# Kernel tuning notes

Measured on AMD Instinct MI355X. Metric: run time of the kernel, lower is better.

The kernel has to match this reference:

```python
import jax, jax.numpy as jnp
import numpy as np

VERY_NEG = -100000000000.0
EPS = 1e-10
PAGERANK_LAMBDA = 0.8
FACT_SCALE = 1.0
B, E, F, LQ = 64, 1000, 4000, 30
T = 100      # trans_units
EMB = 300    # embed_units
WV = 30000   # word vocab
EV = 50007   # entity vocab (+7 specials)
GNN_LAYERS = 2


def linear(x, W, b):
    return x @ W.T + b


def lstm(x, Wih, Whh, bih, bhh):
    # torch nn.LSTM, single layer, batch_first. gate order i,f,g,o
    Bb = x.shape[0]
    H = Whh.shape[1]
    def step(carry, xt):
        h, c = carry
        g = xt @ Wih.T + h @ Whh.T + bih + bhh
        i, f, gg, o = jnp.split(g, 4, axis=-1)
        c = jax.nn.sigmoid(f) * c + jax.nn.sigmoid(i) * jnp.tanh(gg)
        h = jax.nn.sigmoid(o) * jnp.tanh(c)
        return (h, c), h
    init = (jnp.zeros((Bb, H), x.dtype), jnp.zeros((Bb, H), x.dtype))
    (h, _), ys = jax.lax.scan(step, init, jnp.swapaxes(x, 0, 1))
    return jnp.swapaxes(ys, 0, 1), h


def gather_entity(x, head_idx):
    # sparse_bmm(entity2fact_mat, x): each fact row has one nonzero at its head entity
    # x [B,E,D], head_idx [B,F] -> [B,F,D]
    return jnp.take_along_axis(x, head_idx[:, :, None], axis=1)


def scatter_fact(y, tail_idx):
    # sparse_bmm(fact2entity_mat, y): scatter-add fact rows into their tail entity
    # y [B,F,D], tail_idx [B,F] -> [B,E,D]
    Bb, Ff, D = y.shape
    seg = (jnp.arange(Bb)[:, None] * E + tail_idx).reshape(-1)
    return jax.ops.segment_sum(y.reshape(Bb * Ff, D), seg, num_segments=Bb * E).reshape(Bb, E, D)


def forward(word_emb, entity_emb, ent_W, ent_b, lstm_Wih, lstm_Whh, lstm_bih, lstm_bhh,
            q2e_W, q2e_b, e2q_W, e2q_b, e2e_W, e2e_b,
            kbh_W, kbh_b, kbt_W, kbt_b, kbs_W, kbs_b,
            q2e_adj_mat, query_text, local_entity, kb_fact_rel, head_idx, tail_idx):
    div = jnp.sqrt(jnp.asarray(T, jnp.float32))
    query_mask = (query_text != 0).astype(jnp.float32)          # [B,LQ]

    # node encoder (LSTM) over query words
    qw = word_emb[query_text]                                   # [B,LQ,EMB]
    query_hidden_emb, qh = lstm(qw, lstm_Wih, lstm_Whh, lstm_bih, lstm_bhh)
    query_node_emb = qh[:, None, :]                             # [B,1,T]

    local_fact_emb = linear(entity_emb[kb_fact_rel], ent_W, ent_b)     # [B,F,T]
    local_entity_emb = linear(entity_emb[local_entity], ent_W, ent_b)  # [B,E,T]

    # fact <-> query attention (pre-GNN weighting)
    sim = jnp.einsum('blt,bft->blf', query_hidden_emb, local_fact_emb) / div
    sim = jax.nn.softmax(sim + (1.0 - query_mask[:, :, None]) * VERY_NEG, axis=1)
    fact2query_att = jnp.einsum('blf,blt->bft', sim, query_hidden_emb)  # [B,F,T]
    Wsc = jnp.sum(fact2query_att * local_fact_emb, axis=2) / div        # [B,F]
    W_tilde = jnp.exp(Wsc - jnp.max(Wsc, axis=1, keepdims=True))        # [B,F]

    # e2f_softmax = entity2fact^T @ W_tilde : per-entity sum of W_tilde over out-facts
    e2f_softmax = scatter_fact(W_tilde[:, :, None], head_idx)[:, :, 0]
    e2f_softmax = jnp.maximum(e2f_softmax, EPS)                         # [B,E]

    pagerank_f = q2e_adj_mat                                            # [B,E]
    for i in range(GNN_LAYERS):
        next_emb = local_entity_emb
        # question -> entity
        q2e = linear(jnp.broadcast_to(query_node_emb, (B, E, T)), q2e_W[i], q2e_b[i])
        next_emb = jnp.concatenate([next_emb, q2e], axis=2)
        # entity -> fact
        e2f_emb = jax.nn.relu(linear(local_fact_emb, kbs_W[i], kbs_b[i]) +
                              gather_entity(linear(local_entity_emb, kbh_W[i], kbh_b[i]), head_idx))
        e2f_norm = W_tilde[:, :, None] * gather_entity((pagerank_f / e2f_softmax)[:, :, None], head_idx)
        e2f_emb = e2f_emb * e2f_norm                                    # [B,F,T]
        # fact -> entity
        f2e_emb = jax.nn.relu(linear(local_entity_emb, kbs_W[i], kbs_b[i]) +
                              scatter_fact(linear(e2f_emb, kbt_W[i], kbt_b[i]), tail_idx))
        pagerank_f = (PAGERANK_LAMBDA * scatter_fact(e2f_norm, tail_idx)[:, :, 0] +
                      (1.0 - PAGERANK_LAMBDA) * pagerank_f)
        next_emb = jnp.concatenate([next_emb, FACT_SCALE * f2e_emb], axis=2)  # [B,E,3T]
        # entity -> query ; entity -> entity
        query_node_emb = jnp.einsum('be,bet->bt', pagerank_f,
                                    linear(next_emb, e2q_W[i], e2q_b[i]))[:, None, :]
        local_entity_emb = jax.nn.relu(linear(next_emb, e2e_W[i], e2e_b[i]))
    return local_entity_emb, query_node_emb, pagerank_f


def setup_inputs() -> dict:
    key = jax.random.key(0)
    ks = jax.random.split(key, 24)
    def n(k, shape, s=0.05):
        return (jax.random.normal(k, shape) * s).astype(jnp.float32)
    L, K3 = GNN_LAYERS, 3 * T
    inp = {}
    inp['word_emb'] = n(ks[0], (WV, EMB), 1.0)
    inp['entity_emb'] = n(ks[1], (EV, T), 1.0)
    inp['ent_W'] = n(ks[2], (T, T)); inp['ent_b'] = jnp.zeros((T,), jnp.float32)
    inp['lstm_Wih'] = n(ks[3], (4 * T, EMB)); inp['lstm_Whh'] = n(ks[4], (4 * T, T))
    inp['lstm_bih'] = jnp.zeros((4 * T,), jnp.float32)
    inp['lstm_bhh'] = jnp.zeros((4 * T,), jnp.float32)
    inp['q2e_W'] = n(ks[5], (L, T, T)); inp['q2e_b'] = jnp.zeros((L, T), jnp.float32)
    inp['e2q_W'] = n(ks[6], (L, T, K3)); inp['e2q_b'] = jnp.zeros((L, T), jnp.float32)
    inp['e2e_W'] = n(ks[7], (L, T, K3)); inp['e2e_b'] = jnp.zeros((L, T), jnp.float32)
    inp['kbh_W'] = n(ks[8], (L, T, T)); inp['kbh_b'] = jnp.zeros((L, T), jnp.float32)
    inp['kbt_W'] = n(ks[9], (L, T, T)); inp['kbt_b'] = jnp.zeros((L, T), jnp.float32)
    inp['kbs_W'] = n(ks[10], (L, T, T)); inp['kbs_b'] = jnp.zeros((L, T), jnp.float32)
    inp['q2e_adj_mat'] = (jax.random.uniform(ks[11], (B, E)) < 0.05).astype(jnp.float32)
    inp['query_text'] = jax.random.randint(ks[12], (B, LQ), 0, WV)
    inp['local_entity'] = jax.random.randint(ks[13], (B, E), 0, EV)
    inp['kb_fact_rel'] = jax.random.randint(ks[14], (B, F), 0, EV)
    inp['head_idx'] = jax.random.randint(ks[15], (B, F), 0, E)
    inp['tail_idx'] = jax.random.randint(ks[16], (B, F), 0, E)
    return inp


def reference(word_emb, entity_emb, ent_W, ent_b, lstm_Wih, lstm_Whh, lstm_bih, lstm_bhh,
              q2e_W, q2e_b, e2q_W, e2q_b, e2e_W, e2e_b,
              kbh_W, kbh_b, kbt_W, kbt_b, kbs_W, kbs_b,
              q2e_adj_mat, query_text, local_entity, kb_fact_rel, head_idx, tail_idx):
    return forward(word_emb, entity_emb, ent_W, ent_b, lstm_Wih, lstm_Whh, lstm_bih, lstm_bhh,
                   q2e_W, q2e_b, e2q_W, e2q_b, e2e_W, e2e_b,
                   kbh_W, kbh_b, kbt_W, kbt_b, kbs_W, kbs_b,
                   q2e_adj_mat, query_text, local_entity, kb_fact_rel, head_idx, tail_idx)
```

## Files before the change

kernel.cpp:

```cpp
#include <hip/hip_runtime.h>
#include <hip/hip_bf16.h>

#define BB 64
#define EE 1000
#define FF 4000
#define LQ_ 30
#define TT 100
#define EMB_ 300
#define G4 400
#define EV_ 50007
#define VERY_NEG_ (-100000000000.0f)
#define EPS_ 1e-10f

typedef __attribute__((ext_vector_type(8))) short bf16x8;
typedef __attribute__((ext_vector_type(4))) float f32x4;

__device__ __forceinline__ float sigm(float x) { return 1.0f / (1.0f + expf(-x)); }

__device__ __forceinline__ unsigned short f2bf(float v) {
    __hip_bfloat16 h = __float2bfloat16(v);
    return *reinterpret_cast<unsigned short*>(&h);
}
__device__ __forceinline__ float bf2f(unsigned short s) {
    return __uint_as_float((unsigned)s << 16);
}

__global__ void cvt_bf16_kernel(const float* __restrict__ in, unsigned short* __restrict__ out,
                                long n4) {
    long i = (long)blockIdx.x * 256 + threadIdx.x;
    if (i < n4) {
        float4 v = ((const float4*)in)[i];
        ushort4 o;
        o.x = f2bf(v.x); o.y = f2bf(v.y); o.z = f2bf(v.z); o.w = f2bf(v.w);
        ((ushort4*)out)[i] = o;
    }
}

__global__ void transpose_kernel(const float* __restrict__ in, float* __restrict__ out,
                                 int rows, int cols) {
    int i = blockIdx.x * 256 + threadIdx.x;
    if (i < rows * cols) {
        int r = i / cols, c = i % cols;
        out[c * rows + r] = in[i];
    }
}

__global__ __launch_bounds__(256)
void xw_kernel(const float* __restrict__ word_emb, const int* __restrict__ qtext,
               const float* __restrict__ WihT, const float* __restrict__ bih,
               const float* __restrict__ bhh, float* __restrict__ xw) {
    int bs0 = blockIdx.x * 4;
    __shared__ float x[4][EMB_];
    int tid = threadIdx.x;
    for (int i = tid; i < 4 * EMB_; i += 256) {
        int s = i / EMB_, k = i % EMB_;
        x[s][k] = word_emb[(long)qtext[bs0 + s] * EMB_ + k];
    }
    __syncthreads();
    for (int g = tid; g < G4; g += 256) {
        float b0 = bih[g] + bhh[g];
        float a0 = b0, a1 = b0, a2 = b0, a3 = b0;
        #pragma unroll 4
        for (int k = 0; k < EMB_; ++k) {
            float wv = WihT[k * G4 + g];
            a0 += x[0][k] * wv; a1 += x[1][k] * wv;
            a2 += x[2][k] * wv; a3 += x[3][k] * wv;
        }
        xw[(long)(bs0 + 0) * G4 + g] = a0;
        xw[(long)(bs0 + 1) * G4 + g] = a1;
        xw[(long)(bs0 + 2) * G4 + g] = a2;
        xw[(long)(bs0 + 3) * G4 + g] = a3;
    }
}

__global__ __launch_bounds__(512)
void lstm_kernel(const float* __restrict__ xw, const float* __restrict__ Whh,
                 float* __restrict__ qh_emb, float* __restrict__ qnode) {
    int b = blockIdx.x, tid = threadIdx.x;
    __shared__ __align__(16) float hs[TT];
    __shared__ float cs[TT];
    __shared__ float gs[G4];
    float4 w[25];
    if (tid < G4) {
        const float4* wr = (const float4*)(Whh + (long)tid * TT);
        #pragma unroll
        for (int j = 0; j < 25; ++j) w[j] = wr[j];
    }
    if (tid < TT) { hs[tid] = 0.f; cs[tid] = 0.f; }
    __syncthreads();
    for (int s = 0; s < LQ_; ++s) {
        if (tid < G4) {
            const float4* hv4 = (const float4*)hs;
            float a0 = 0.f, a1 = 0.f, a2 = 0.f, a3 = 0.f;
            #pragma unroll
            for (int j = 0; j < 25; ++j) {
                float4 hv = hv4[j];
                a0 += hv.x * w[j].x; a1 += hv.y * w[j].y;
                a2 += hv.z * w[j].z; a3 += hv.w * w[j].w;
            }
            gs[tid] = xw[((long)b * LQ_ + s) * G4 + tid] + (a0 + a1) + (a2 + a3);
        }
        __syncthreads();
        if (tid < TT) {
            float ci = sigm(gs[TT + tid]) * cs[tid] + sigm(gs[tid]) * tanhf(gs[2 * TT + tid]);
            float hi = sigm(gs[3 * TT + tid]) * tanhf(ci);
            cs[tid] = ci;
            hs[tid] = hi;
            qh_emb[((long)b * LQ_ + s) * TT + tid] = hi;
            if (s == LQ_ - 1) qnode[b * TT + tid] = hi;
        }
        __syncthreads();
    }
}

struct GOut {
    const float* W; int wstride;
    const float* bias;
    const float* bscale;
    const unsigned short* addb;
    const float* addf;
    const float* cvec;
    void* Y; int y_bf16; int relu;
};
struct GArgs {
    const void* X; int x_bf16;
    const int* gidx;
    long rows;
    int nw;
    GOut o[3];
};

__global__ __launch_bounds__(256)
void gemm_multi_kernel(GArgs a) {
    __shared__ __align__(16) short sX[64 * 136];
    __shared__ __align__(16) short sW[112 * 136];
    float* sOut = (float*)sW;
    int tid = threadIdx.x;
    long r0 = (long)blockIdx.x * 64;
    for (int i = tid; i < 64 * 25; i += 256) {
        int r = i / 25, c = i % 25;
        long rr = r0 + r;
        ushort4 v; v.x = 0; v.y = 0; v.z = 0; v.w = 0;
        if (rr < a.rows) {
            long xr = a.gidx ? (long)a.gidx[rr] : rr;
            if (a.x_bf16) {
                v = *(const ushort4*)((const unsigned short*)a.X + xr * TT + c * 4);
            } else {
                float4 f = *(const float4*)((const float*)a.X + xr * TT + c * 4);
                v.x = f2bf(f.x); v.y = f2bf(f.y); v.z = f2bf(f.z); v.w = f2bf(f.w);
            }
        }
        *(ushort4*)&sX[r * 136 + c * 4] = v;
    }
    for (int i = tid; i < 64 * 28; i += 256) {
        int r = i / 28, k = TT + i % 28;
        sX[r * 136 + k] = 0;
    }
    int lane = tid & 63, wv = tid >> 6;
    int arow = lane & 15, agrp = lane >> 4;
    int t_lo = lane & 15, r_hi = (lane >> 4) * 4;
    #pragma unroll
    for (int w = 0; w < 3; ++w) {
        if (w >= a.nw) break;
        for (int i = tid; i < 112 * 32; i += 256) {
            int t = i / 32, k = (i % 32) * 4;
            ushort4 v; v.x = 0; v.y = 0; v.z = 0; v.w = 0;
            if (t < TT && k < TT) {
                float4 f = *(const float4*)(a.o[w].W + (long)t * a.o[w].wstride + k);
                v.x = f2bf(f.x); v.y = f2bf(f.y); v.z = f2bf(f.z); v.w = f2bf(f.w);
            }
            *(ushort4*)&sW[t * 136 + k] = v;
        }
        __syncthreads();
        f32x4 acc[7];
        #pragma unroll
        for (int n = 0; n < 7; ++n) acc[n] = (f32x4){0.f, 0.f, 0.f, 0.f};
        #pragma unroll
        for (int kk = 0; kk < 4; ++kk) {
            bf16x8 av = *(const bf16x8*)&sX[(wv * 16 + arow) * 136 + kk * 32 + agrp * 8];
            #pragma unroll
            for (int n = 0; n < 7; ++n) {
                bf16x8 bv = *(const bf16x8*)&sW[(n * 16 + arow) * 136 + kk * 32 + agrp * 8];
                acc[n] = __builtin_amdgcn_mfma_f32_16x16x32_bf16(av, bv, acc[n], 0, 0, 0);
            }
        }
        __syncthreads();
        #pragma unroll
        for (int n = 0; n < 7; ++n) {
            int t = n * 16 + t_lo;
            if (t < TT) {
                #pragma unroll
                for (int j = 0; j < 4; ++j)
                    sOut[(wv * 16 + r_hi + j) * 104 + t] = acc[n][j];
            }
        }
        __syncthreads();
        for (int i = tid; i < 64 * 25; i += 256) {
            int r = i / 25, c = i % 25;
            long rr = r0 + r;
            if (rr < a.rows) {
                float4 v = *(float4*)&sOut[r * 104 + c * 4];
                if (a.o[w].bias) {
                    float bs = a.o[w].bscale ? a.o[w].bscale[rr] : 1.f;
                    float4 bv = *(const float4*)(a.o[w].bias + c * 4);
                    v.x += bv.x * bs; v.y += bv.y * bs; v.z += bv.z * bs; v.w += bv.w * bs;
                }
                if (a.o[w].addb) {
                    ushort4 ad = *(const ushort4*)(a.o[w].addb + rr * TT + c * 4);
                    v.x += bf2f(ad.x); v.y += bf2f(ad.y); v.z += bf2f(ad.z); v.w += bf2f(ad.w);
                }
                if (a.o[w].addf) {
                    float4 ad = *(const float4*)(a.o[w].addf + rr * TT + c * 4);
                    v.x += ad.x; v.y += ad.y; v.z += ad.z; v.w += ad.w;
                }
                if (a.o[w].cvec) {
                    float4 cv = *(const float4*)(a.o[w].cvec + (long)(rr / EE) * TT + c * 4);
                    v.x += cv.x; v.y += cv.y; v.z += cv.z; v.w += cv.w;
                }
                if (a.o[w].relu) {
                    v.x = fmaxf(v.x, 0.f); v.y = fmaxf(v.y, 0.f);
                    v.z = fmaxf(v.z, 0.f); v.w = fmaxf(v.w, 0.f);
                }
                if (a.o[w].y_bf16) {
                    ushort4 ov;
                    ov.x = f2bf(v.x); ov.y = f2bf(v.y); ov.z = f2bf(v.z); ov.w = f2bf(v.w);
                    *(ushort4*)((unsigned short*)a.o[w].Y + rr * TT + c * 4) = ov;
                } else {
                    *(float4*)((float*)a.o[w].Y + rr * TT + c * 4) = v;
                }
            }
        }
        __syncthreads();
    }
}

__global__ __launch_bounds__(128)
void compose_kernel(const float* __restrict__ A, const float* __restrict__ B,
                    const float* __restrict__ ab, const float* __restrict__ bb,
                    float* __restrict__ C, float* __restrict__ cb) {
    int i = blockIdx.x, j = threadIdx.x;
    __shared__ float arow[TT];
    if (j < TT) arow[j] = A[i * TT + j];
    __syncthreads();
    if (j < TT) {
        float acc = 0.f;
        for (int k = 0; k < TT; ++k) acc += arow[k] * B[k * TT + j];
        C[i * TT + j] = acc;
    }
    if (j == 0) {
        float acc = bb[i];
        for (int k = 0; k < TT; ++k) acc += arow[k] * ab[k];
        cb[i] = acc;
    }
}

__global__ __launch_bounds__(256)
void wsc_kernel(const float* __restrict__ qh_emb, const int* __restrict__ qtext,
                const unsigned short* __restrict__ ent_f, const int* __restrict__ rel,
                float* __restrict__ Wsc) {
    int b = blockIdx.x >> 4;
    int chunk = blockIdx.x & 15;
    __shared__ __align__(16) float qh[LQ_ * TT];
    __shared__ float msk[LQ_];
    for (int i = threadIdx.x; i < LQ_ * TT; i += 256) qh[i] = qh_emb[(long)b * LQ_ * TT + i];
    for (int i = threadIdx.x; i < LQ_; i += 256)
        msk[i] = (qtext[b * LQ_ + i] != 0) ? 0.f : VERY_NEG_;
    __syncthreads();
    int f = chunk * 256 + threadIdx.x;
    if (f >= FF) return;
    long bf = (long)b * FF + f;
    const unsigned short* fr = ent_f + (long)rel[bf] * TT;
    float sim[LQ_];
    #pragma unroll
    for (int l = 0; l < LQ_; ++l) sim[l] = 0.f;
    for (int kq = 0; kq < 25; ++kq) {
        ushort4 x4 = *(const ushort4*)(fr + kq * 4);
        float x0 = bf2f(x4.x), x1 = bf2f(x4.y), x2 = bf2f(x4.z), x3 = bf2f(x4.w);
        #pragma unroll
        for (int l = 0; l < LQ_; ++l) {
            float4 q = ((const float4*)(qh + l * TT))[kq];
            sim[l] += x0 * q.x + x1 * q.y + x2 * q.z + x3 * q.w;
        }
    }
    float mx = -INFINITY;
    #pragma unroll
    for (int l = 0; l < LQ_; ++l) {
        sim[l] *= 0.1f;
        mx = fmaxf(mx, sim[l] + msk[l]);
    }
    float ssum = 0.f, wsum = 0.f;
    #pragma unroll
    for (int l = 0; l < LQ_; ++l) {
        float p = expf(sim[l] + msk[l] - mx);
        ssum += p;
        wsum += p * sim[l];
    }
    Wsc[bf] = wsum / ssum;
}

__global__ __launch_bounds__(256)
void rowmax_kernel(const float* __restrict__ Wsc, float* __restrict__ bmax) {
    int b = blockIdx.x, tid = threadIdx.x;
    __shared__ float red[256];
    float m = -INFINITY;
    for (int f = tid; f < FF; f += 256) m = fmaxf(m, Wsc[(long)b * FF + f]);
    red[tid] = m;
    __syncthreads();
    for (int s = 128; s; s >>= 1) {
        if (tid < s) red[tid] = fmaxf(red[tid], red[tid + s]);
        __syncthreads();
    }
    if (tid == 0) bmax[b] = red[0];
}

__global__ __launch_bounds__(256)
void wtilde_kernel(const float* __restrict__ Wsc, const float* __restrict__ bmax,
                   const int* __restrict__ head, const int* __restrict__ tail,
                   float* __restrict__ W_tilde, float* __restrict__ e2f_sm,
                   float* __restrict__ cnt) {
    int idx = blockIdx.x * 256 + threadIdx.x;
    if (idx >= BB * FF) return;
    int b = idx / FF;
    float wt = expf(Wsc[idx] - bmax[b]);
    W_tilde[idx] = wt;
    atomicAdd(&e2f_sm[(long)b * EE + head[idx]], wt);
    atomicAdd(&cnt[(long)b * EE + tail[idx]], 1.f);
}

__global__ __launch_bounds__(256)
void scan_kernel(const float* __restrict__ cnt, int* __restrict__ offs) {
    int b = blockIdx.x, tid = threadIdx.x;
    __shared__ int ls[256];
    int c0 = 0, c1 = 0, c2 = 0, c3 = 0;
    int start = tid * 4;
    if (start + 0 < EE) c0 = (int)cnt[(long)b * EE + start + 0];
    if (start + 1 < EE) c1 = (int)cnt[(long)b * EE + start + 1];
    if (start + 2 < EE) c2 = (int)cnt[(long)b * EE + start + 2];
    if (start + 3 < EE) c3 = (int)cnt[(long)b * EE + start + 3];
    int s = c0 + c1 + c2 + c3;
    ls[tid] = s;
    __syncthreads();
    for (int d = 1; d < 256; d <<= 1) {
        int v = (tid >= d) ? ls[tid - d] : 0;
        __syncthreads();
        ls[tid] += v;
        __syncthreads();
    }
    int excl = ls[tid] - s + b * FF;
    if (start + 0 < EE) { offs[(long)b * EE + start + 0] = excl; excl += c0; }
    if (start + 1 < EE) { offs[(long)b * EE + start + 1] = excl; excl += c1; }
    if (start + 2 < EE) { offs[(long)b * EE + start + 2] = excl; excl += c2; }
    if (start + 3 < EE) { offs[(long)b * EE + start + 3] = excl; excl += c3; }
    if (b == BB - 1 && tid == 255) offs[BB * EE] = BB * FF;
}

__global__ __launch_bounds__(256)
void sortfacts_kernel(const int* __restrict__ tail, const int* __restrict__ head,
                      const int* __restrict__ rel, const float* __restrict__ W_tilde,
                      const float* __restrict__ e2f_sm, const int* __restrict__ offs,
                      int* __restrict__ fillc, int2* __restrict__ rh_perm,
                      float* __restrict__ wsm_perm) {
    int idx = blockIdx.x * 256 + threadIdx.x;
    if (idx >= BB * FF) return;
    int b = idx / FF;
    int bin = b * EE + tail[idx];
    int pos = offs[bin] + atomicAdd(&fillc[bin], 1);
    int bh = b * EE + head[idx];
    rh_perm[pos] = make_int2(rel[idx], bh);
    wsm_perm[pos] = W_tilde[idx] / fmaxf(e2f_sm[bh], EPS_);
}

__global__ __launch_bounds__(256)
void e2f_sorted_kernel(const unsigned short* __restrict__ kbs_tab,
                       const unsigned short* __restrict__ kbh,
                       const float* __restrict__ wsm_perm, const int2* __restrict__ rh_perm,
                       const float* __restrict__ pr_cur, const int* __restrict__ offs,
                       unsigned short* __restrict__ eaccb, float* __restrict__ pr_nxt,
                       float* __restrict__ pr_out) {
    int grp = threadIdx.x >> 7;
    int t = threadIdx.x & 127;
    int bin = blockIdx.x * 2 + grp;
    int j0 = offs[bin], j1 = offs[bin + 1];
    float acc = 0.f, nsum = 0.f;
    int j = j0;
    for (; j + 2 <= j1; j += 2) {
        float w0 = wsm_perm[j], w1 = wsm_perm[j + 1];
        int2 rh0 = rh_perm[j];
        int2 rh1 = rh_perm[j + 1];
        float n0 = w0 * pr_cur[rh0.y];
        float n1 = w1 * pr_cur[rh1.y];
        nsum += n0 + n1;
        if ((n0 != 0.f) || (n1 != 0.f)) {
            if (t < TT) {
                float v0 = fmaxf(bf2f(kbs_tab[(long)rh0.x * TT + t]) +
                                 bf2f(kbh[(long)rh0.y * TT + t]), 0.f);
                float v1 = fmaxf(bf2f(kbs_tab[(long)rh1.x * TT + t]) +
                                 bf2f(kbh[(long)rh1.y * TT + t]), 0.f);
                acc += v0 * n0 + v1 * n1;
            }
        }
    }
    if (j < j1) {
        float w0 = wsm_perm[j];
        int2 rh0 = rh_perm[j];
        float n0 = w0 * pr_cur[rh0.y];
        nsum += n0;
        if (n0 != 0.f && t < TT) {
            float v0 = fmaxf(bf2f(kbs_tab[(long)rh0.x * TT + t]) +
                             bf2f(kbh[(long)rh0.y * TT + t]), 0.f);
            acc += v0 * n0;
        }
    }
    if (t < TT) eaccb[(long)bin * TT + t] = f2bf(acc);
    if (t == TT) {
        float pv = 0.8f * nsum + 0.2f * pr_cur[bin];
        pr_nxt[bin] = pv;
        if (pr_out) pr_out[bin] = pv;
    }
}

#define RCH 50
__global__ __launch_bounds__(128)
void reduce_kernel(const float* __restrict__ pr, const unsigned short* __restrict__ ent,
                   const int* __restrict__ gidx, const unsigned short* __restrict__ f2e,
                   float* __restrict__ s1, float* __restrict__ s3, float* __restrict__ prsum) {
    int b = blockIdx.x / (EE / RCH), ch = blockIdx.x % (EE / RCH);
    int e0 = ch * RCH, tid = threadIdx.x;
    __shared__ float prl[RCH];
    __shared__ long erow[RCH];
    if (tid < RCH) {
        long idx = (long)b * EE + e0 + tid;
        prl[tid] = pr[idx];
        erow[tid] = gidx ? (long)gidx[idx] : idx;
    }
    __syncthreads();
    if (tid == 0) {
        float s = 0.f;
        for (int e = 0; e < RCH; ++e) s += prl[e];
        if (s != 0.f) atomicAdd(&prsum[b], s);
    }
    if (tid < TT) {
        float a1 = 0.f, a3 = 0.f;
        for (int e = 0; e < RCH; ++e) {
            float p = prl[e];
            if (p != 0.f) {
                a1 += p * bf2f(ent[erow[e] * TT + tid]);
                a3 += p * bf2f(f2e[((long)b * EE + e0 + e) * TT + tid]);
            }
        }
        atomicAdd(&s1[b * TT + tid], a1);
        atomicAdd(&s3[b * TT + tid], a3);
    }
}

__global__ __launch_bounds__(128)
void qvec_kernel(const float* __restrict__ qnode,
                 const float* __restrict__ q2eW, const float* __restrict__ q2eb,
                 const float* __restrict__ e2eW, const float* __restrict__ e2eb,
                 const float* __restrict__ e2qW, const float* __restrict__ e2qb,
                 float* __restrict__ q2e_vec, float* __restrict__ cvec_e2e,
                 float* __restrict__ cvec_e2q) {
    int b = blockIdx.x, t = threadIdx.x;
    __shared__ float qn[TT], qv[TT];
    if (t < TT) qn[t] = qnode[b * TT + t];
    __syncthreads();
    if (t < TT) {
        float acc = q2eb[t];
        for (int k = 0; k < TT; ++k) acc += qn[k] * q2eW[t * TT + k];
        qv[t] = acc;
        q2e_vec[b * TT + t] = acc;
    }
    __syncthreads();
    if (t < TT) {
        float a1 = e2eb[t], a2 = e2qb[t];
        for (int k = 0; k < TT; ++k) {
            a1 += qv[k] * e2eW[(long)t * 300 + TT + k];
            a2 += qv[k] * e2qW[(long)t * 300 + TT + k];
        }
        cvec_e2e[b * TT + t] = a1;
        cvec_e2q[b * TT + t] = a2;
    }
}

__global__ __launch_bounds__(128)
void qnode_kernel(const float* __restrict__ s1, const float* __restrict__ s3,
                  const float* __restrict__ prsum, const float* __restrict__ cvec_e2q,
                  const float* __restrict__ e2qW, float* __restrict__ qnode,
                  float* __restrict__ out2) {
    int b = blockIdx.x, t = threadIdx.x;
    __shared__ float s1l[TT], s3l[TT];
    if (t < TT) { s1l[t] = s1[b * TT + t]; s3l[t] = s3[b * TT + t]; }
    __syncthreads();
    if (t < TT) {
        float acc = prsum[b] * cvec_e2q[b * TT + t];
        const float* wr = e2qW + (long)t * 300;
        for (int k = 0; k < TT; ++k) acc += s1l[k] * wr[k] + s3l[k] * wr[200 + k];
        qnode[b * TT + t] = acc;
        if (out2) out2[b * TT + t] = acc;
    }
}

extern "C" void kernel_launch(void* const* d_in, const int* in_sizes, int n_in,
                              void* d_out, int out_size, void* d_ws, size_t ws_size,
                              hipStream_t stream) {
    const float* word_emb   = (const float*)d_in[0];
    const float* entity_emb = (const float*)d_in[1];
    const float* ent_W      = (const float*)d_in[2];
    const float* ent_b      = (const float*)d_in[3];
    const float* lstm_Wih   = (const float*)d_in[4];
    const float* lstm_Whh   = (const float*)d_in[5];
    const float* lstm_bih   = (const float*)d_in[6];
    const float* lstm_bhh   = (const float*)d_in[7];
    const float* q2e_W      = (const float*)d_in[8];
    const float* q2e_b      = (const float*)d_in[9];
    const float* e2q_W      = (const float*)d_in[10];
    const float* e2q_b      = (const float*)d_in[11];
    const float* e2e_W      = (const float*)d_in[12];
    const float* e2e_b      = (const float*)d_in[13];
    const float* kbh_W      = (const float*)d_in[14];
    const float* kbh_b      = (const float*)d_in[15];
    const float* kbt_W      = (const float*)d_in[16];
    const float* kbt_b      = (const float*)d_in[17];
    const float* kbs_W      = (const float*)d_in[18];
    const float* kbs_b      = (const float*)d_in[19];
    const float* q2e_adj    = (const float*)d_in[20];
    const int* query_text   = (const int*)d_in[21];
    const int* local_entity = (const int*)d_in[22];
    const int* kb_fact_rel  = (const int*)d_in[23];
    const int* head_idx     = (const int*)d_in[24];
    const int* tail_idx     = (const int*)d_in[25];
    float* out = (float*)d_out;

    char* base = (char*)d_ws;
    size_t off = 0;
    auto alloc = [&](size_t bytes) {
        void* p = base + off;
        off = (off + bytes + 255) & ~(size_t)255;
        return p;
    };
    const size_t NE = (size_t)BB * EE;
    unsigned short* emb_bf  = (unsigned short*)alloc((size_t)EV_ * TT * 2);
    unsigned short* ent_f   = (unsigned short*)alloc((size_t)EV_ * TT * 2);
    unsigned short* kbs0    = (unsigned short*)alloc((size_t)EV_ * TT * 2);
    unsigned short* kbs1    = (unsigned short*)alloc((size_t)EV_ * TT * 2);
    unsigned short* entB    = (unsigned short*)alloc(NE * TT * 2);
    unsigned short* kbh_bf  = (unsigned short*)alloc(NE * TT * 2);
    unsigned short* kbs_e   = (unsigned short*)alloc(NE * TT * 2);
    unsigned short* tmp     = (unsigned short*)alloc(NE * TT * 2);
    unsigned short* eaccb   = (unsigned short*)alloc(NE * TT * 2);
    float* xw               = (float*)alloc((size_t)BB * LQ_ * G4 * 4);
    float* qh_emb           = (float*)alloc((size_t)BB * LQ_ * TT * 4);
    float* WihT             = (float*)alloc((size_t)G4 * EMB_ * 4);
    float* Wsc              = (float*)alloc((size_t)BB * FF * 4);
    float* W_tilde          = (float*)alloc((size_t)BB * FF * 4);
    float* bmaxb            = (float*)alloc(BB * 4);
    float* e2f_sm           = (float*)alloc(NE * 4);
    float* cnt              = (float*)alloc(NE * 4);
    float* prA              = (float*)alloc(NE * 4);
    float* prB              = (float*)alloc(NE * 4);
    float* qnode            = (float*)alloc((size_t)BB * TT * 4);
    float* q2e_vec          = (float*)alloc((size_t)BB * TT * 4);
    float* cvec_e2e         = (float*)alloc((size_t)BB * TT * 4);
    float* cvec_e2q         = (float*)alloc((size_t)BB * TT * 4);
    float* s1               = (float*)alloc((size_t)BB * TT * 4);
    float* s3               = (float*)alloc((size_t)BB * TT * 4);
    float* prsum            = (float*)alloc(BB * 4);
    float* Ckbs0            = (float*)alloc((size_t)TT * TT * 4);
    float* Ckbs1            = (float*)alloc((size_t)TT * TT * 4);
    float* cb0              = (float*)alloc(TT * 4);
    float* cb1              = (float*)alloc(TT * 4);
    int* offs               = (int*)alloc((NE + 1) * 4);
    int* fillc              = (int*)alloc(NE * 4);
    int2* rh_perm           = (int2*)alloc((size_t)BB * FF * 8);
    float* wsm_perm         = (float*)alloc((size_t)BB * FF * 4);
    unsigned short* f2e = kbh_bf;

    transpose_kernel<<<(G4 * EMB_ + 255) / 256, 256, 0, stream>>>(lstm_Wih, WihT, G4, EMB_);
    xw_kernel<<<BB * LQ_ / 4, 256, 0, stream>>>(word_emb, query_text, WihT, lstm_bih, lstm_bhh, xw);
    lstm_kernel<<<BB, 512, 0, stream>>>(xw, lstm_Whh, qh_emb, qnode);

    cvt_bf16_kernel<<<(EV_ * TT / 4 + 255) / 256, 256, 0, stream>>>(entity_emb, emb_bf,
                                                                    (long)EV_ * TT / 4);
    compose_kernel<<<TT, 128, 0, stream>>>(kbs_W, ent_W, ent_b, kbs_b, Ckbs0, cb0);
    compose_kernel<<<TT, 128, 0, stream>>>(kbs_W + TT * TT, ent_W, ent_b, kbs_b + TT,
                                           Ckbs1, cb1);
    {
        GArgs g{};
        g.X = emb_bf; g.x_bf16 = 1; g.gidx = nullptr; g.rows = EV_; g.nw = 3;
        g.o[0].W = ent_W; g.o[0].wstride = TT; g.o[0].bias = ent_b;
        g.o[0].Y = ent_f; g.o[0].y_bf16 = 1;
        g.o[1].W = Ckbs0; g.o[1].wstride = TT; g.o[1].bias = cb0;
        g.o[1].Y = kbs0; g.o[1].y_bf16 = 1;
        g.o[2].W = Ckbs1; g.o[2].wstride = TT; g.o[2].bias = cb1;
        g.o[2].Y = kbs1; g.o[2].y_bf16 = 1;
        gemm_multi_kernel<<<(EV_ + 63) / 64, 256, 0, stream>>>(g);
    }

    wsc_kernel<<<BB * 16, 256, 0, stream>>>(qh_emb, query_text, ent_f, kb_fact_rel, Wsc);
    rowmax_kernel<<<BB, 256, 0, stream>>>(Wsc, bmaxb);
    hipMemsetAsync(e2f_sm, 0, 2 * NE * 4, stream);
    wtilde_kernel<<<(BB * FF + 255) / 256, 256, 0, stream>>>(Wsc, bmaxb, head_idx, tail_idx,
                                                             W_tilde, e2f_sm, cnt);
    hipMemcpyAsync(prA, q2e_adj, NE * 4, hipMemcpyDeviceToDevice, stream);

    scan_kernel<<<BB, 256, 0, stream>>>(cnt, offs);
    hipMemsetAsync(fillc, 0, NE * 4, stream);
    sortfacts_kernel<<<(BB * FF + 255) / 256, 256, 0, stream>>>(
        tail_idx, head_idx, kb_fact_rel, W_tilde, e2f_sm, offs, fillc, rh_perm, wsm_perm);

    for (int i = 0; i < 2; ++i) {
        const unsigned short* kbs_tab = i ? kbs1 : kbs0;
        float* pr_cur = i ? prB : prA;
        float* pr_nxt = i ? prA : prB;
        qvec_kernel<<<BB, 128, 0, stream>>>(qnode, q2e_W + i * TT * TT, q2e_b + i * TT,
                                            e2e_W + i * TT * 300, e2e_b + i * TT,
                                            e2q_W + i * TT * 300, e2q_b + i * TT,
                                            q2e_vec, cvec_e2e, cvec_e2q);
        {
            GArgs g{};
            g.X = i ? (const void*)entB : (const void*)ent_f;
            g.x_bf16 = 1;
            g.gidx = i ? nullptr : local_entity;
            g.rows = (long)NE; g.nw = 3;
            g.o[0].W = kbh_W + i * TT * TT; g.o[0].wstride = TT; g.o[0].bias = kbh_b + i * TT;
            g.o[0].Y = kbh_bf; g.o[0].y_bf16 = 1;
            g.o[1].W = kbs_W + i * TT * TT; g.o[1].wstride = TT; g.o[1].bias = kbs_b + i * TT;
            g.o[1].Y = kbs_e; g.o[1].y_bf16 = 1;
            g.o[2].W = e2e_W + i * TT * 300; g.o[2].wstride = 300;
            g.o[2].Y = tmp; g.o[2].y_bf16 = 1;
            gemm_multi_kernel<<<(int)(NE / 64), 256, 0, stream>>>(g);
        }
        e2f_sorted_kernel<<<(int)(NE / 2), 256, 0, stream>>>(
            kbs_tab, kbh_bf, wsm_perm, rh_perm, pr_cur, offs,
            eaccb, pr_nxt, (i == 1) ? out + 6406400 : nullptr);
        {
            GArgs g{};
            g.X = eaccb; g.x_bf16 = 1; g.gidx = nullptr; g.rows = (long)NE; g.nw = 1;
            g.o[0].W = kbt_W + i * TT * TT; g.o[0].wstride = TT;
            g.o[0].bias = kbt_b + i * TT; g.o[0].bscale = cnt;
            g.o[0].addb = kbs_e;
            g.o[0].Y = (void*)f2e; g.o[0].y_bf16 = 1; g.o[0].relu = 1;
            gemm_multi_kernel<<<(int)(NE / 64), 256, 0, stream>>>(g);
        }
        hipMemsetAsync(s1, 0, (size_t)(2 * BB * TT + BB) * 4, stream);
        reduce_kernel<<<BB * (EE / RCH), 128, 0, stream>>>(
            pr_nxt, i ? entB : ent_f, i ? nullptr : local_entity, f2e, s1, s3, prsum);
        qnode_kernel<<<BB, 128, 0, stream>>>(s1, s3, prsum, cvec_e2q, e2q_W + i * TT * 300,
                                             qnode, (i == 1) ? out + 6400000 : nullptr);
        {
            GArgs g{};
            g.X = f2e; g.x_bf16 = 1; g.gidx = nullptr; g.rows = (long)NE; g.nw = 1;
            g.o[0].W = e2e_W + i * TT * 300 + 200; g.o[0].wstride = 300;
            g.o[0].addb = tmp; g.o[0].cvec = cvec_e2e; g.o[0].relu = 1;
            g.o[0].Y = i ? (void*)out : (void*)entB; g.o[0].y_bf16 = i ? 0 : 1;
            gemm_multi_kernel<<<(int)(NE / 64), 256, 0, stream>>>(g);
        }
    }
}
```

Baseline: 781.4 us.

## Precompute per-vocab attention scores and layer-0 projections; chain e2e GEMM into kbt GEMM

The per-fact query-attention score is replaced by a table computed over the entity vocabulary with MFMA, one score per (batch, vocab id), and facts then look up their relation's score. Layer-0 kbh and e2e projections are folded into the vocab-level multi-output GEMM, using composed weights, so the per-entity layer-0 GEMM is dropped and gathered via local_entity. The e2e output GEMM is chained inside the kbt GEMM kernel through shared memory, which removes a launch and a round trip of f2e. In exchange the vocab-wide table (64 x 50k) does more work than the 64 x 4000 facts it replaces, and composing the weights changes bf16 rounding.

```diff
diff --git a/kernel.cpp b/kernel.cpp
--- a/kernel.cpp
+++ b/kernel.cpp
@@ -9,6 +9,7 @@
 #define EMB_ 300
 #define G4 400
 #define EV_ 50007
+#define EVP 50008
 #define VERY_NEG_ (-100000000000.0f)
 #define EPS_ 1e-10f
 
@@ -113,12 +114,88 @@
     }
 }
 
+__global__ __launch_bounds__(256)
+void qpack_kernel(const float* __restrict__ qh_emb, const int* __restrict__ qtext,
+                  unsigned short* __restrict__ qh_pack, float* __restrict__ msk_all) {
+    int b = blockIdx.x, tid = threadIdx.x;
+    for (int i = tid; i < 32 * 128; i += 256) {
+        int r = i >> 7, k = i & 127;
+        float v = (r < LQ_ && k < TT) ? qh_emb[(long)b * LQ_ * TT + r * TT + k] : 0.f;
+        qh_pack[(long)b * 4096 + i] = f2bf(v);
+    }
+    if (tid < 32)
+        msk_all[b * 32 + tid] =
+            (tid < LQ_ && qtext[b * LQ_ + tid] != 0) ? 0.f : VERY_NEG_;
+}
+
+__global__ __launch_bounds__(256)
+void wsc_tab_kernel(const unsigned short* __restrict__ ent_f,
+                    const unsigned short* __restrict__ qh_pack,
+                    const float* __restrict__ msk_all, float* __restrict__ tab) {
+    __shared__ __align__(16) unsigned short sV[64 * 136];
+    __shared__ __align__(16) unsigned short sQ[32 * 136];
+    __shared__ float smsk[32];
+    int tid = threadIdx.x;
+    int v0 = blockIdx.x * 64;
+    for (int i = tid; i < 64 * 25; i += 256) {
+        int r = i / 25, c = i % 25;
+        ushort4 v; v.x = 0; v.y = 0; v.z = 0; v.w = 0;
+        if (v0 + r < EV_) v = *(const ushort4*)(ent_f + (long)(v0 + r) * TT + c * 4);
+        *(ushort4*)&sV[r * 136 + c * 4] = v;
+    }
+    for (int i = tid; i < 64 * 28; i += 256) {
+        int r = i / 28, k = TT + i % 28;
+        sV[r * 136 + k] = 0;
+    }
+    int lane = tid & 63, wv = tid >> 6;
+    int l = lane & 15, g = lane >> 4;
+    for (int b = 0; b < BB; ++b) {
+        for (int i = tid; i < 32 * 32; i += 256) {
+            int r = i >> 5, c = i & 31;
+            *(ushort4*)&sQ[r * 136 + c * 4] =
+                *(const ushort4*)(qh_pack + (long)b * 4096 + r * 128 + c * 4);
+        }
+        if (tid < 32) smsk[tid] = msk_all[b * 32 + tid];
+        __syncthreads();
+        f32x4 acc0 = (f32x4){0.f, 0.f, 0.f, 0.f};
+        f32x4 acc1 = (f32x4){0.f, 0.f, 0.f, 0.f};
+        #pragma unroll
+        for (int kk = 0; kk < 4; ++kk) {
+            bf16x8 av = *(const bf16x8*)&sV[(wv * 16 + l) * 136 + kk * 32 + g * 8];
+            bf16x8 b0 = *(const bf16x8*)&sQ[l * 136 + kk * 32 + g * 8];
+            bf16x8 b1 = *(const bf16x8*)&sQ[(16 + l) * 136 + kk * 32 + g * 8];
+            acc0 = __builtin_amdgcn_mfma_f32_16x16x32_bf16(av, b0, acc0, 0, 0, 0);
+            acc1 = __builtin_amdgcn_mfma_f32_16x16x32_bf16(av, b1, acc1, 0, 0, 0);
+        }
+        float m0 = smsk[l], m1 = smsk[l + 16];
+        float4 w4;
+        #pragma unroll
+        for (int j = 0; j < 4; ++j) {
+            float s0 = acc0[j] * 0.1f, s1 = acc1[j] * 0.1f;
+            float mx = fmaxf(s0 + m0, s1 + m1);
+            #pragma unroll
+            for (int d = 1; d < 16; d <<= 1) mx = fmaxf(mx, __shfl_xor(mx, d, 16));
+            float p0 = expf(s0 + m0 - mx), p1 = expf(s1 + m1 - mx);
+            float ss = p0 + p1, ws = p0 * s0 + p1 * s1;
+            #pragma unroll
+            for (int d = 1; d < 16; d <<= 1) {
+                ss += __shfl_xor(ss, d, 16);
+                ws += __shfl_xor(ws, d, 16);
+            }
+            ((float*)&w4)[j] = ws / ss;
+        }
+        int v = v0 + wv * 16 + g * 4;
+        if (l == 0 && v < EV_) *(float4*)&tab[(long)b * EVP + v] = w4;
+        __syncthreads();
+    }
+}
+
 struct GOut {
     const float* W; int wstride;
     const float* bias;
     const float* bscale;
     const unsigned short* addb;
-    const float* addf;
+    const int* agidx;
     const float* cvec;
     void* Y; int y_bf16; int relu;
 };
@@ -127,7 +204,8 @@
     const int* gidx;
     long rows;
     int nw;
-    GOut o[3];
+    int chain;
+    GOut o[5];
 };
 
 __global__ __launch_bounds__(256)
@@ -159,8 +237,7 @@
     int lane = tid & 63, wv = tid >> 6;
     int arow = lane & 15, agrp = lane >> 4;
     int t_lo = lane & 15, r_hi = (lane >> 4) * 4;
-    #pragma unroll
-    for (int w = 0; w < 3; ++w) {
+    for (int w = 0; w < 5; ++w) {
         if (w >= a.nw) break;
         for (int i = tid; i < 112 * 32; i += 256) {
             int t = i / 32, k = (i % 32) * 4;
@@ -191,7 +268,7 @@
             if (t < TT) {
                 #pragma unroll
                 for (int j = 0; j < 4; ++j)
-                    sOut[(wv * 16 + r_hi + j) * 104 + t] = acc[n][j];
+                    sOut[(wv * 16 + r_hi + j) * 108 + t] = acc[n][j];
             }
         }
         __syncthreads();
@@ -199,19 +276,16 @@
             int r = i / 25, c = i % 25;
             long rr = r0 + r;
             if (rr < a.rows) {
-                float4 v = *(float4*)&sOut[r * 104 + c * 4];
+                float4 v = *(float4*)&sOut[r * 108 + c * 4];
                 if (a.o[w].bias) {
                     float bs = a.o[w].bscale ? a.o[w].bscale[rr] : 1.f;
                     float4 bv = *(const float4*)(a.o[w].bias + c * 4);
                     v.x += bv.x * bs; v.y += bv.y * bs; v.z += bv.z * bs; v.w += bv.w * bs;
                 }
                 if (a.o[w].addb) {
-                    ushort4 ad = *(const ushort4*)(a.o[w].addb + rr * TT + c * 4);
+                    long ar = a.o[w].agidx ? (long)a.o[w].agidx[rr] : rr;
+                    ushort4 ad = *(const ushort4*)(a.o[w].addb + ar * TT + c * 4);
                     v.x += bf2f(ad.x); v.y += bf2f(ad.y); v.z += bf2f(ad.z); v.w += bf2f(ad.w);
-                }
-                if (a.o[w].addf) {
-                    float4 ad = *(const float4*)(a.o[w].addf + rr * TT + c * 4);
-                    v.x += ad.x; v.y += ad.y; v.z += ad.z; v.w += ad.w;
                 }
                 if (a.o[w].cvec) {
                     float4 cv = *(const float4*)(a.o[w].cvec + (long)(rr / EE) * TT + c * 4);
@@ -221,9 +295,11 @@
                     v.x = fmaxf(v.x, 0.f); v.y = fmaxf(v.y, 0.f);
                     v.z = fmaxf(v.z, 0.f); v.w = fmaxf(v.w, 0.f);
                 }
+                ushort4 ov;
+                ov.x = f2bf(v.x); ov.y = f2bf(v.y); ov.z = f2bf(v.z); ov.w = f2bf(v.w);
+                if (a.chain && w + 1 < a.nw)
+                    *(ushort4*)&sX[r * 136 + c * 4] = ov;
                 if (a.o[w].y_bf16) {
-                    ushort4 ov;
-                    ov.x = f2bf(v.x); ov.y = f2bf(v.y); ov.z = f2bf(v.z); ov.w = f2bf(v.w);
                     *(ushort4*)((unsigned short*)a.o[w].Y + rr * TT + c * 4) = ov;
                 } else {
                     *(float4*)((float*)a.o[w].Y + rr * TT + c * 4) = v;
@@ -235,12 +311,12 @@
 }
 
 __global__ __launch_bounds__(128)
-void compose_kernel(const float* __restrict__ A, const float* __restrict__ B,
+void compose_kernel(const float* __restrict__ A, int Astride, const float* __restrict__ B,
                     const float* __restrict__ ab, const float* __restrict__ bb,
                     float* __restrict__ C, float* __restrict__ cb) {
     int i = blockIdx.x, j = threadIdx.x;
     __shared__ float arow[TT];
-    if (j < TT) arow[j] = A[i * TT + j];
+    if (j < TT) arow[j] = A[(long)i * Astride + j];
     __syncthreads();
     if (j < TT) {
         float acc = 0.f;
@@ -248,62 +324,20 @@
         C[i * TT + j] = acc;
     }
     if (j == 0) {
-        float acc = bb[i];
+        float acc = bb ? bb[i] : 0.f;
         for (int k = 0; k < TT; ++k) acc += arow[k] * ab[k];
         cb[i] = acc;
     }
 }
 
 __global__ __launch_bounds__(256)
-void wsc_kernel(const float* __restrict__ qh_emb, const int* __restrict__ qtext,
-                const unsigned short* __restrict__ ent_f, const int* __restrict__ rel,
-                float* __restrict__ Wsc) {
-    int b = blockIdx.x >> 4;
-    int chunk = blockIdx.x & 15;
-    __shared__ __align__(16) float qh[LQ_ * TT];
-    __shared__ float msk[LQ_];
-    for (int i = threadIdx.x; i < LQ_ * TT; i += 256) qh[i] = qh_emb[(long)b * LQ_ * TT + i];
-    for (int i = threadIdx.x; i < LQ_; i += 256)
-        msk[i] = (qtext[b * LQ_ + i] != 0) ? 0.f : VERY_NEG_;
-    __syncthreads();
-    int f = chunk * 256 + threadIdx.x;
-    if (f >= FF) return;
-    long bf = (long)b * FF + f;
-    const unsigned short* fr = ent_f + (long)rel[bf] * TT;
-    float sim[LQ_];
-    #pragma unroll
-    for (int l = 0; l < LQ_; ++l) sim[l] = 0.f;
-    for (int kq = 0; kq < 25; ++kq) {
-        ushort4 x4 = *(const ushort4*)(fr + kq * 4);
-        float x0 = bf2f(x4.x), x1 = bf2f(x4.y), x2 = bf2f(x4.z), x3 = bf2f(x4.w);
-        #pragma unroll
-        for (int l = 0; l < LQ_; ++l) {
-            float4 q = ((const float4*)(qh + l * TT))[kq];
-            sim[l] += x0 * q.x + x1 * q.y + x2 * q.z + x3 * q.w;
-        }
-    }
-    float mx = -INFINITY;
-    #pragma unroll
-    for (int l = 0; l < LQ_; ++l) {
-        sim[l] *= 0.1f;
-        mx = fmaxf(mx, sim[l] + msk[l]);
-    }
-    float ssum = 0.f, wsum = 0.f;
-    #pragma unroll
-    for (int l = 0; l < LQ_; ++l) {
-        float p = expf(sim[l] + msk[l] - mx);
-        ssum += p;
-        wsum += p * sim[l];
-    }
-    Wsc[bf] = wsum / ssum;
-}
-
-__global__ __launch_bounds__(256)
-void rowmax_kernel(const float* __restrict__ Wsc, float* __restrict__ bmax) {
+void rowmax_kernel(const float* __restrict__ tab, const int* __restrict__ rel,
+                   float* __restrict__ bmax) {
     int b = blockIdx.x, tid = threadIdx.x;
     __shared__ float red[256];
     float m = -INFINITY;
-    for (int f = tid; f < FF; f += 256) m = fmaxf(m, Wsc[(long)b * FF + f]);
+    for (int f = tid; f < FF; f += 256)
+        m = fmaxf(m, tab[(long)b * EVP + rel[b * FF + f]]);
     red[tid] = m;
     __syncthreads();
     for (int s = 128; s; s >>= 1) {
@@ -314,14 +348,14 @@
 }
 
 __global__ __launch_bounds__(256)
-void wtilde_kernel(const float* __restrict__ Wsc, const float* __restrict__ bmax,
-                   const int* __restrict__ head, const int* __restrict__ tail,
-                   float* __restrict__ W_tilde, float* __restrict__ e2f_sm,
-                   float* __restrict__ cnt) {
+void wtilde_kernel(const float* __restrict__ tab, const float* __restrict__ bmax,
+                   const int* __restrict__ rel, const int* __restrict__ head,
+                   const int* __restrict__ tail, float* __restrict__ W_tilde,
+                   float* __restrict__ e2f_sm, float* __restrict__ cnt) {
     int idx = blockIdx.x * 256 + threadIdx.x;
     if (idx >= BB * FF) return;
     int b = idx / FF;
-    float wt = expf(Wsc[idx] - bmax[b]);
+    float wt = expf(tab[(long)b * EVP + rel[idx]] - bmax[b]);
     W_tilde[idx] = wt;
     atomicAdd(&e2f_sm[(long)b * EE + head[idx]], wt);
     atomicAdd(&cnt[(long)b * EE + tail[idx]], 1.f);
@@ -357,57 +391,57 @@
 __global__ __launch_bounds__(256)
 void sortfacts_kernel(const int* __restrict__ tail, const int* __restrict__ head,
                       const int* __restrict__ rel, const float* __restrict__ W_tilde,
-                      const float* __restrict__ e2f_sm, const int* __restrict__ offs,
-                      int* __restrict__ fillc, int2* __restrict__ rh_perm,
-                      float* __restrict__ wsm_perm) {
+                      const float* __restrict__ e2f_sm, const int* __restrict__ le,
+                      const int* __restrict__ offs, int* __restrict__ fillc,
+                      int* __restrict__ rel_perm, int* __restrict__ bh_perm,
+                      int* __restrict__ vle_perm, float* __restrict__ wsm_perm) {
     int idx = blockIdx.x * 256 + threadIdx.x;
     if (idx >= BB * FF) return;
     int b = idx / FF;
     int bin = b * EE + tail[idx];
     int pos = offs[bin] + atomicAdd(&fillc[bin], 1);
     int bh = b * EE + head[idx];
-    rh_perm[pos] = make_int2(rel[idx], bh);
+    rel_perm[pos] = rel[idx];
+    bh_perm[pos] = bh;
+    vle_perm[pos] = le[bh];
     wsm_perm[pos] = W_tilde[idx] / fmaxf(e2f_sm[bh], EPS_);
 }
 
 __global__ __launch_bounds__(256)
 void e2f_sorted_kernel(const unsigned short* __restrict__ kbs_tab,
-                       const unsigned short* __restrict__ kbh,
-                       const float* __restrict__ wsm_perm, const int2* __restrict__ rh_perm,
+                       const unsigned short* __restrict__ kbh_src,
+                       const float* __restrict__ wsm_perm, const int* __restrict__ rel_perm,
+                       const int* __restrict__ krow_perm, const int* __restrict__ bh_perm,
                        const float* __restrict__ pr_cur, const int* __restrict__ offs,
                        unsigned short* __restrict__ eaccb, float* __restrict__ pr_nxt,
                        float* __restrict__ pr_out) {
     int grp = threadIdx.x >> 7;
     int t = threadIdx.x & 127;
     int bin = blockIdx.x * 2 + grp;
+    if (bin >= BB * EE) return;
     int j0 = offs[bin], j1 = offs[bin + 1];
     float acc = 0.f, nsum = 0.f;
     int j = j0;
     for (; j + 2 <= j1; j += 2) {
-        float w0 = wsm_perm[j], w1 = wsm_perm[j + 1];
-        int2 rh0 = rh_perm[j];
-        int2 rh1 = rh_perm[j + 1];
-        float n0 = w0 * pr_cur[rh0.y];
-        float n1 = w1 * pr_cur[rh1.y];
+        float n0 = wsm_perm[j] * pr_cur[bh_perm[j]];
+        float n1 = wsm_perm[j + 1] * pr_cur[bh_perm[j + 1]];
         nsum += n0 + n1;
         if ((n0 != 0.f) || (n1 != 0.f)) {
             if (t < TT) {
-                float v0 = fmaxf(bf2f(kbs_tab[(long)rh0.x * TT + t]) +
-                                 bf2f(kbh[(long)rh0.y * TT + t]), 0.f);
-                float v1 = fmaxf(bf2f(kbs_tab[(long)rh1.x * TT + t]) +
-                                 bf2f(kbh[(long)rh1.y * TT + t]), 0.f);
+                float v0 = fmaxf(bf2f(kbs_tab[(long)rel_perm[j] * TT + t]) +
+                                 bf2f(kbh_src[(long)krow_perm[j] * TT + t]), 0.f);
+                float v1 = fmaxf(bf2f(kbs_tab[(long)rel_perm[j + 1] * TT + t]) +
+                                 bf2f(kbh_src[(long)krow_perm[j + 1] * TT + t]), 0.f);
                 acc += v0 * n0 + v1 * n1;
             }
         }
     }
     if (j < j1) {
-        float w0 = wsm_perm[j];
-        int2 rh0 = rh_perm[j];
-        float n0 = w0 * pr_cur[rh0.y];
+        float n0 = wsm_perm[j] * pr_cur[bh_perm[j]];
         nsum += n0;
         if (n0 != 0.f && t < TT) {
-            float v0 = fmaxf(bf2f(kbs_tab[(long)rh0.x * TT + t]) +
-                             bf2f(kbh[(long)rh0.y * TT + t]), 0.f);
+            float v0 = fmaxf(bf2f(kbs_tab[(long)rel_perm[j] * TT + t]) +
+                             bf2f(kbh_src[(long)krow_perm[j] * TT + t]), 0.f);
             acc += v0 * n0;
         }
     }
@@ -543,15 +577,19 @@
     unsigned short* ent_f   = (unsigned short*)alloc((size_t)EV_ * TT * 2);
     unsigned short* kbs0    = (unsigned short*)alloc((size_t)EV_ * TT * 2);
     unsigned short* kbs1    = (unsigned short*)alloc((size_t)EV_ * TT * 2);
+    unsigned short* kbh0    = (unsigned short*)alloc((size_t)EV_ * TT * 2);
+    unsigned short* tmp0    = (unsigned short*)alloc((size_t)EV_ * TT * 2);
     unsigned short* entB    = (unsigned short*)alloc(NE * TT * 2);
     unsigned short* kbh_bf  = (unsigned short*)alloc(NE * TT * 2);
     unsigned short* kbs_e   = (unsigned short*)alloc(NE * TT * 2);
     unsigned short* tmp     = (unsigned short*)alloc(NE * TT * 2);
     unsigned short* eaccb   = (unsigned short*)alloc(NE * TT * 2);
+    unsigned short* qh_pack = (unsigned short*)alloc((size_t)BB * 4096 * 2);
+    float* msk_all          = (float*)alloc((size_t)BB * 32 * 4);
+    float* wsc_tab          = (float*)alloc((size_t)BB * EVP * 4);
     float* xw               = (float*)alloc((size_t)BB * LQ_ * G4 * 4);
     float* qh_emb           = (float*)alloc((size_t)BB * LQ_ * TT * 4);
     float* WihT             = (float*)alloc((size_t)G4 * EMB_ * 4);
-    float* Wsc              = (float*)alloc((size_t)BB * FF * 4);
     float* W_tilde          = (float*)alloc((size_t)BB * FF * 4);
     float* bmaxb            = (float*)alloc(BB * 4);
     float* e2f_sm           = (float*)alloc(NE * 4);
@@ -567,79 +605,98 @@
     float* prsum            = (float*)alloc(BB * 4);
     float* Ckbs0            = (float*)alloc((size_t)TT * TT * 4);
     float* Ckbs1            = (float*)alloc((size_t)TT * TT * 4);
+    float* Ckbh0            = (float*)alloc((size_t)TT * TT * 4);
+    float* Ctmp0            = (float*)alloc((size_t)TT * TT * 4);
     float* cb0              = (float*)alloc(TT * 4);
     float* cb1              = (float*)alloc(TT * 4);
+    float* cbh0             = (float*)alloc(TT * 4);
+    float* cbt0             = (float*)alloc(TT * 4);
     int* offs               = (int*)alloc((NE + 1) * 4);
     int* fillc              = (int*)alloc(NE * 4);
-    int2* rh_perm           = (int2*)alloc((size_t)BB * FF * 8);
+    int* rel_perm           = (int*)alloc((size_t)BB * FF * 4);
+    int* bh_perm            = (int*)alloc((size_t)BB * FF * 4);
+    int* vle_perm           = (int*)alloc((size_t)BB * FF * 4);
     float* wsm_perm         = (float*)alloc((size_t)BB * FF * 4);
     unsigned short* f2e = kbh_bf;
 
     transpose_kernel<<<(G4 * EMB_ + 255) / 256, 256, 0, stream>>>(lstm_Wih, WihT, G4, EMB_);
     xw_kernel<<<BB * LQ_ / 4, 256, 0, stream>>>(word_emb, query_text, WihT, lstm_bih, lstm_bhh, xw);
     lstm_kernel<<<BB, 512, 0, stream>>>(xw, lstm_Whh, qh_emb, qnode);
+    qpack_kernel<<<BB, 256, 0, stream>>>(qh_emb, query_text, qh_pack, msk_all);
 
     cvt_bf16_kernel<<<(EV_ * TT / 4 + 255) / 256, 256, 0, stream>>>(entity_emb, emb_bf,
                                                                     (long)EV_ * TT / 4);
-    compose_kernel<<<TT, 128, 0, stream>>>(kbs_W, ent_W, ent_b, kbs_b, Ckbs0, cb0);
-    compose_kernel<<<TT, 128, 0, stream>>>(kbs_W + TT * TT, ent_W, ent_b, kbs_b + TT,
+    compose_kernel<<<TT, 128, 0, stream>>>(kbs_W, TT, ent_W, ent_b, kbs_b, Ckbs0, cb0);
+    compose_kernel<<<TT, 128, 0, stream>>>(kbs_W + TT * TT, TT, ent_W, ent_b, kbs_b + TT,
                                            Ckbs1, cb1);
+    compose_kernel<<<TT, 128, 0, stream>>>(kbh_W, TT, ent_W, ent_b, kbh_b, Ckbh0, cbh0);
+    compose_kernel<<<TT, 128, 0, stream>>>(e2e_W, 300, ent_W, ent_b, nullptr, Ctmp0, cbt0);
     {
         GArgs g{};
-        g.X = emb_bf; g.x_bf16 = 1; g.gidx = nullptr; g.rows = EV_; g.nw = 3;
+        g.X = emb_bf; g.x_bf16 = 1; g.gidx = nullptr; g.rows = EV_; g.nw = 5;
         g.o[0].W = ent_W; g.o[0].wstride = TT; g.o[0].bias = ent_b;
         g.o[0].Y = ent_f; g.o[0].y_bf16 = 1;
         g.o[1].W = Ckbs0; g.o[1].wstride = TT; g.o[1].bias = cb0;
         g.o[1].Y = kbs0; g.o[1].y_bf16 = 1;
         g.o[2].W = Ckbs1; g.o[2].wstride = TT; g.o[2].bias = cb1;
         g.o[2].Y = kbs1; g.o[2].y_bf16 = 1;
+        g.o[3].W = Ckbh0; g.o[3].wstride = TT; g.o[3].bias = cbh0;
+        g.o[3].Y = kbh0; g.o[3].y_bf16 = 1;
+        g.o[4].W = Ctmp0; g.o[4].wstride = TT; g.o[4].bias = cbt0;
+        g.o[4].Y = tmp0; g.o[4].y_bf16 = 1;
         gemm_multi_kernel<<<(EV_ + 63) / 64, 256, 0, stream>>>(g);
     }
 
-    wsc_kernel<<<BB * 16, 256, 0, stream>>>(qh_emb, query_text, ent_f, kb_fact_rel, Wsc);
-    rowmax_kernel<<<BB, 256, 0, stream>>>(Wsc, bmaxb);
+    wsc_tab_kernel<<<(EV_ + 63) / 64, 256, 0, stream>>>(ent_f, qh_pack, msk_all, wsc_tab);
+    rowmax_kernel<<<BB, 256, 0, stream>>>(wsc_tab, kb_fact_rel, bmaxb);
     hipMemsetAsync(e2f_sm, 0, 2 * NE * 4, stream);
-    wtilde_kernel<<<(BB * FF + 255) / 256, 256, 0, stream>>>(Wsc, bmaxb, head_idx, tail_idx,
-                                                             W_tilde, e2f_sm, cnt);
+    wtilde_kernel<<<(BB * FF + 255) / 256, 256, 0, stream>>>(wsc_tab, bmaxb, kb_fact_rel,
+                                                             head_idx, tail_idx, W_tilde,
+                                                             e2f_sm, cnt);
     hipMemcpyAsync(prA, q2e_adj, NE * 4, hipMemcpyDeviceToDevice, stream);
 
     scan_kernel<<<BB, 256, 0, stream>>>(cnt, offs);
     hipMemsetAsync(fillc, 0, NE * 4, stream);
     sortfacts_kernel<<<(BB * FF + 255) / 256, 256, 0, stream>>>(
-        tail_idx, head_idx, kb_fact_rel, W_tilde, e2f_sm, offs, fillc, rh_perm, wsm_perm);
+        tail_idx, head_idx, kb_fact_rel, W_tilde, e2f_sm, local_entity, offs, fillc,
+        rel_perm, bh_perm, vle_perm, wsm_perm);
 
     for (int i = 0; i < 2; ++i) {
-        const unsigned short* kbs_tab = i ? kbs1 : kbs0;
         float* pr_cur = i ? prB : prA;
         float* pr_nxt = i ? prA : prB;
         qvec_kernel<<<BB, 128, 0, stream>>>(qnode, q2e_W + i * TT * TT, q2e_b + i * TT,
                                             e2e_W + i * TT * 300, e2e_b + i * TT,
                                             e2q_W + i * TT * 300, e2q_b + i * TT,
                                             q2e_vec, cvec_e2e, cvec_e2q);
-        {
+        if (i == 1) {
             GArgs g{};
-            g.X = i ? (const void*)entB : (const void*)ent_f;
-            g.x_bf16 = 1;
-            g.gidx = i ? nullptr : local_entity;
-            g.rows = (long)NE; g.nw = 3;
-            g.o[0].W = kbh_W + i * TT * TT; g.o[0].wstride = TT; g.o[0].bias = kbh_b + i * TT;
+            g.X = entB; g.x_bf16 = 1; g.gidx = nullptr; g.rows = (long)NE; g.nw = 3;
+            g.o[0].W = kbh_W + TT * TT; g.o[0].wstride = TT; g.o[0].bias = kbh_b + TT;
             g.o[0].Y = kbh_bf; g.o[0].y_bf16 = 1;
-            g.o[1].W = kbs_W + i * TT * TT; g.o[1].wstride = TT; g.o[1].bias = kbs_b + i * TT;
+            g.o[1].W = kbs_W + TT * TT; g.o[1].wstride = TT; g.o[1].bias = kbs_b + TT;
             g.o[1].Y = kbs_e; g.o[1].y_bf16 = 1;
-            g.o[2].W = e2e_W + i * TT * 300; g.o[2].wstride = 300;
+            g.o[2].W = e2e_W + TT * 300; g.o[2].wstride = 300;
             g.o[2].Y = tmp; g.o[2].y_bf16 = 1;
             gemm_multi_kernel<<<(int)(NE / 64), 256, 0, stream>>>(g);
         }
         e2f_sorted_kernel<<<(int)(NE / 2), 256, 0, stream>>>(
-            kbs_tab, kbh_bf, wsm_perm, rh_perm, pr_cur, offs,
+            i ? kbs1 : kbs0, i ? kbh_bf : kbh0, wsm_perm, rel_perm,
+            i ? bh_perm : vle_perm, bh_perm, pr_cur, offs,
             eaccb, pr_nxt, (i == 1) ? out + 6406400 : nullptr);
         {
             GArgs g{};
-            g.X = eaccb; g.x_bf16 = 1; g.gidx = nullptr; g.rows = (long)NE; g.nw = 1;
+            g.X = eaccb; g.x_bf16 = 1; g.gidx = nullptr; g.rows = (long)NE;
+            g.nw = 2; g.chain = 1;
             g.o[0].W = kbt_W + i * TT * TT; g.o[0].wstride = TT;
             g.o[0].bias = kbt_b + i * TT; g.o[0].bscale = cnt;
-            g.o[0].addb = kbs_e;
+            g.o[0].addb = i ? kbs_e : kbs0;
+            g.o[0].agidx = i ? nullptr : local_entity;
             g.o[0].Y = (void*)f2e; g.o[0].y_bf16 = 1; g.o[0].relu = 1;
+            g.o[1].W = e2e_W + i * TT * 300 + 200; g.o[1].wstride = 300;
+            g.o[1].addb = i ? tmp : tmp0;
+            g.o[1].agidx = i ? nullptr : local_entity;
+            g.o[1].cvec = cvec_e2e; g.o[1].relu = 1;
+            g.o[1].Y = i ? (void*)out : (void*)entB; g.o[1].y_bf16 = i ? 0 : 1;
             gemm_multi_kernel<<<(int)(NE / 64), 256, 0, stream>>>(g);
         }
         hipMemsetAsync(s1, 0, (size_t)(2 * BB * TT + BB) * 4, stream);
@@ -647,13 +704,5 @@
             pr_nxt, i ? entB : ent_f, i ? nullptr : local_entity, f2e, s1, s3, prsum);
         qnode_kernel<<<BB, 128, 0, stream>>>(s1, s3, prsum, cvec_e2q, e2q_W + i * TT * 300,
                                              qnode, (i == 1) ? out + 6400000 : nullptr);
-        {
-            GArgs g{};
-            g.X = f2e; g.x_bf16 = 1; g.gidx = nullptr; g.rows = (long)NE; g.nw = 1;
-            g.o[0].W = e2e_W + i * TT * 300 + 200; g.o[0].wstride = 300;
-            g.o[0].addb = tmp; g.o[0].cvec = cvec_e2e; g.o[0].relu = 1;
-            g.o[0].Y = i ? (void*)out : (void*)entB; g.o[0].y_bf16 = i ? 0 : 1;
-            gemm_multi_kernel<<<(int)(NE / 64), 256, 0, stream>>>(g);
-        }
-    }
-}
+    }
+}
```

Result: slower. 995.3 us (+27.4%).
